# Kernel optimization log

Measured on AMD Instinct MI355X. Metric: run time of the kernel, lower is better.

The kernel has to match this reference:

```python
import jax, jax.numpy as jnp
import numpy as np

# dims
B, N, T, D = 32, 207, 12, 128
H, HD, L, FF = 8, 16, 4, 512
PL, OD, IN = 12, 1, 1
SCALE = 1.0 / float(np.sqrt(HD))
NEG = -1e9


def ln(x, g, b, eps=1e-5):
    m = jnp.mean(x, -1, keepdims=True)
    v = jnp.mean((x - m) ** 2, -1, keepdims=True)
    return (x - m) * jax.lax.rsqrt(v + eps) * g + b


def setup_inputs() -> dict:
    key = jax.random.key(0)
    keys = iter(jax.random.split(key, 48))
    def rn(shape, s=0.02):
        return jax.random.normal(next(keys), shape, jnp.float32) * s
    z = lambda *s: jnp.zeros(s, jnp.float32)
    o = lambda *s: jnp.ones(s, jnp.float32)
    inp = {
        "x": jax.random.normal(next(keys), (B, N, T, IN), jnp.float32),
        "adj": jax.random.randint(next(keys), (N, N), 0, 2, jnp.int32),
        "Wi": rn((IN, D)), "bi": z(D),
        # spatial blocks (stacked over L layers)
        "Wq": rn((L, D, D)), "Wk": rn((L, D, D)), "Wv": rn((L, D, D)),
        "Wo": rn((L, D, D)), "bo": z(L, D),
        "sW1": rn((L, D, FF)), "sB1": z(L, FF), "sW2": rn((L, FF, D)), "sB2": z(L, D),
        "sg1": o(L, D), "sh1": z(L, D), "sg2": o(L, D), "sh2": z(L, D),
        # temporal blocks
        "Win": rn((L, D, 3 * D)), "Bin": z(L, 3 * D), "Wout": rn((L, D, D)), "Bout": z(L, D),
        "tW1": rn((L, D, FF)), "tB1": z(L, FF), "tW2": rn((L, FF, D)), "tB2": z(L, D),
        "tg1": o(L, D), "th1": z(L, D), "tg2": o(L, D), "th2": z(L, D),
        # prediction head
        "P1": rn((D, 2 * D)), "Pb1": z(2 * D), "P2": rn((2 * D, D)), "Pb2": z(D),
        "P3": rn((D, PL * OD)), "Pb3": z(PL * OD),
    }
    return inp


def reference(x, adj, Wi, bi, Wq, Wk, Wv, Wo, bo, sW1, sB1, sW2, sB2,
              sg1, sh1, sg2, sh2, Win, Bin, Wout, Bout, tW1, tB1, tW2, tB2,
              tg1, th1, tg2, th2, P1, Pb1, P2, Pb2, P3, Pb3):
    mask = (adj == 0)  # [N,N] True = masked (no edge)
    cmask = jnp.triu(jnp.ones((T, T), bool), 1)  # causal mask over time
    h = x @ Wi + bi  # [B,N,T,D]
    for l in range(L):
        # --- spatial adjacency-masked attention (vectorized over t) ---
        xn = ln(h, sg1[l], sh1[l])
        q = (xn @ Wq[l]).reshape(B, N, T, H, HD)
        k = (xn @ Wk[l]).reshape(B, N, T, H, HD)
        v = (xn @ Wv[l]).reshape(B, N, T, H, HD)
        sc = jnp.einsum('bnthd,bmthd->bthnm', q, k) * SCALE  # [B,T,H,N,N]
        sc = jnp.where(mask[None, None, None], NEG, sc)
        a = jax.nn.softmax(sc, -1)
        o = jnp.einsum('bthnm,bmthd->bnthd', a, v).reshape(B, N, T, D)
        h = h + o @ Wo[l] + bo[l]
        xn = ln(h, sg2[l], sh2[l])
        h = h + jax.nn.relu(xn @ sW1[l] + sB1[l]) @ sW2[l] + sB2[l]
        # --- temporal causal attention (per node) ---
        xn = ln(h, tg1[l], th1[l])
        qkv = xn @ Win[l] + Bin[l]
        q, k, v = jnp.split(qkv, 3, -1)
        q = q.reshape(B, N, T, H, HD)
        k = k.reshape(B, N, T, H, HD)
        v = v.reshape(B, N, T, H, HD)
        sc = jnp.einsum('bnthd,bnshd->bnhts', q, k) * SCALE  # [B,N,H,T,T]
        sc = jnp.where(cmask[None, None, None], NEG, sc)
        a = jax.nn.softmax(sc, -1)
        o = jnp.einsum('bnhts,bnshd->bnthd', a, v).reshape(B, N, T, D)
        h = h + o @ Wout[l] + Bout[l]
        xn = ln(h, tg2[l], th2[l])
        h = h + jax.nn.relu(xn @ tW1[l] + tB1[l]) @ tW2[l] + tB2[l]
    # prediction head on last time step
    hl = h[:, :, -1, :]  # [B,N,D]
    zz = jax.nn.relu(hl @ P1 + Pb1)
    zz = jax.nn.relu(zz @ P2 + Pb2)
    return (zz @ P3 + Pb3).reshape(B, N, PL, OD)
```

## Files before the change

### kernel.cpp

```cpp
#include <hip/hip_runtime.h>
#include <hip/hip_bf16.h>

#define B_   32
#define N_   207
#define T_   12
#define D_   128
#define H_   8
#define HD_  16
#define L_   4
#define FF_  512
#define PL_  12
#define TOK  (B_*N_*T_)
#define ROWS2 (B_*N_)
#define SCALE_ 0.25f
#define NEG_  -1e9f
#define NPAD 208
#define KQ2  24
#define KVH  232
#define SLAB 3312
#define MSK_N (13*13*256)

typedef __hip_bfloat16 bf16;
typedef unsigned int u32;
typedef __attribute__((ext_vector_type(4))) unsigned int u32x4;
typedef __attribute__((ext_vector_type(8))) short bf16x8;
typedef __attribute__((ext_vector_type(8))) _Float16 f16x8;
typedef __attribute__((ext_vector_type(4))) float f32x4;

__device__ __forceinline__ float b2f(bf16 x){ return __bfloat162float(x); }
__device__ __forceinline__ bf16  f2b(float x){ return __float2bfloat16(x); }

__device__ __forceinline__ void gll16(const bf16* g, bf16* l){
  __builtin_amdgcn_global_load_lds((const __attribute__((address_space(1))) void*)g,
                                   (__attribute__((address_space(3))) void*)l, 16, 0, 0);
}

__global__ void detect_k(const void* x, int* flag){
  __shared__ int cnt[256];
  const unsigned short* u = (const unsigned short*)x;
  int ok = 0;
  for (int i = threadIdx.x; i < 4096; i += 256){
    unsigned int bits = ((unsigned int)u[i]) << 16;
    float f = __uint_as_float(bits);
    float a = fabsf(f);
    if (f == 0.0f || (a > 1e-4f && a < 64.0f)) ok++;
  }
  cnt[threadIdx.x] = ok;
  __syncthreads();
  for (int s = 128; s > 0; s >>= 1){
    if (threadIdx.x < s) cnt[threadIdx.x] += cnt[threadIdx.x + s];
    __syncthreads();
  }
  if (threadIdx.x == 0) *flag = (cnt[0] > 3686) ? 1 : 0;
}

struct FlatArgs {
  const void* src[24];
  long long dst[24];
  int cum[25];
};
__global__ void cvt_flat_k(FlatArgs a, bf16* base, const int* flag, int total){
  int i = blockIdx.x*256 + threadIdx.x;
  if (i >= total) return;
  int j = 0;
  while (i >= a.cum[j+1]) j++;
  int loc = i - a.cum[j];
  float v = (*flag) ? b2f(((const bf16*)a.src[j])[loc]) : ((const float*)a.src[j])[loc];
  base[a.dst[j] + loc] = f2b(v);
}

struct TArgs {
  const void* src[10];
  long long dst[10];
  int K[10], Nc[10], Lstr[10], ro[10];
  float scale[10];
  int cum[11];
};
__global__ void cvt_t_k(TArgs a, bf16* base, const int* flag, int total){
  int i = blockIdx.x*256 + threadIdx.x;
  if (i >= total) return;
  int j = 0;
  while (i >= a.cum[j+1]) j++;
  int loc = i - a.cum[j];
  int KN = a.K[j]*a.Nc[j];
  int l = loc / KN; int rm = loc - l*KN; int k = rm / a.Nc[j]; int n = rm - k*a.Nc[j];
  float v = (*flag) ? b2f(((const bf16*)a.src[j])[loc]) : ((const float*)a.src[j])[loc];
  base[a.dst[j] + (long long)l*a.Lstr[j] + (long long)(a.ro[j]+n)*a.K[j] + k] = f2b(v*a.scale[j]);
}

__global__ void maskc_k(const int* adj, float* maskg){
  int i = blockIdx.x*256 + threadIdx.x;
  if (i >= MSK_N) return;
  int cell = i >> 8;
  int mi = cell / 13, nj = cell - mi*13;
  int rem = i & 255;
  int lane = rem >> 2, r = rem & 3;
  int quad = lane >> 4, cl = lane & 15;
  int row = mi*16 + quad*4 + r; if (row > 206) row = 206;
  int col = nj*16 + cl;
  float v;
  if (col > 206) v = -1e30f;
  else v = adj[row*N_ + col] ? 0.0f : NEG_;
  maskg[i] = v;
}

__global__ void embed_ln_k(const bf16* x, const bf16* Wi, const bf16* bi,
                           const bf16* g, const bf16* bta, float* h, bf16* xnb){
  int wave = threadIdx.x >> 6, lane = threadIdx.x & 63;
  int tok = blockIdx.x*4 + wave;
  if (tok >= TOK) return;
  float xv = b2f(x[tok]);
  float v0 = xv*b2f(Wi[lane])    + b2f(bi[lane]);
  float v1 = xv*b2f(Wi[lane+64]) + b2f(bi[lane+64]);
  float* hp = h + (size_t)tok*D_;
  hp[lane] = v0; hp[lane+64] = v1;
  float s = v0 + v1;
  for (int off = 32; off >= 1; off >>= 1) s += __shfl_xor(s, off, 64);
  float m = s * (1.0f/128.0f);
  float d0 = v0 - m, d1 = v1 - m;
  float vv = d0*d0 + d1*d1;
  for (int off = 32; off >= 1; off >>= 1) vv += __shfl_xor(vv, off, 64);
  float r = rsqrtf(vv*(1.0f/128.0f) + 1e-5f);
  bf16* op = xnb + (size_t)tok*D_;
  op[lane]    = f2b(d0*r*b2f(g[lane])    + b2f(bta[lane]));
  op[lane+64] = f2b(d1*r*b2f(g[lane+64]) + b2f(bta[lane+64]));
}

__global__ __launch_bounds__(256) void mgemm_k(const bf16* __restrict__ A,
    const bf16* __restrict__ Wt, const bf16* __restrict__ bias,
    bf16* __restrict__ outp, int ldo, int Ktot, int relu){
  __shared__ __align__(16) bf16 As[128*32];
  __shared__ __align__(16) bf16 Bs[128*32];
  int tid = threadIdx.x;
  int rowBase = blockIdx.y * 128, colBase = blockIdx.x * 128;
  int w = tid >> 6, lane = tid & 63, quad = lane >> 4, cl = lane & 15;
  int waveM = w >> 1, waveN = w & 1;
  f32x4 accr[4][4];
  #pragma unroll
  for (int i = 0; i < 4; i++)
    #pragma unroll
    for (int j = 0; j < 4; j++) accr[i][j] = (f32x4){0.f,0.f,0.f,0.f};
  int lr = tid >> 2, kc = tid & 3;
  const bf16* Ap = A  + (size_t)(rowBase + lr)*Ktot + kc*8;
  const bf16* Bp = Wt + (size_t)(colBase + lr)*Ktot + kc*8;
  bf16* AsW = As + tid*8;
  bf16* BsW = Bs + tid*8;
  for (int kk = 0; kk < Ktot; kk += 32){
    __syncthreads();
    gll16(Ap + kk, AsW);
    gll16(Ap + (size_t)64*Ktot + kk, AsW + 64*32);
    gll16(Bp + kk, BsW);
    gll16(Bp + (size_t)64*Ktot + kk, BsW + 64*32);
    __syncthreads();
    bf16x8 af[4], bfr[4];
    #pragma unroll
    for (int mi = 0; mi < 4; mi++)
      af[mi] = *(const bf16x8*)(As + (waveM*64 + mi*16 + cl)*32 + quad*8);
    #pragma unroll
    for (int nj = 0; nj < 4; nj++)
      bfr[nj] = *(const bf16x8*)(Bs + (waveN*64 + nj*16 + cl)*32 + quad*8);
    #pragma unroll
    for (int mi = 0; mi < 4; mi++)
      #pragma unroll
      for (int nj = 0; nj < 4; nj++)
        accr[mi][nj] = __builtin_amdgcn_mfma_f32_16x16x32_bf16(af[mi], bfr[nj], accr[mi][nj], 0,0,0);
  }
  float bv[4];
  #pragma unroll
  for (int nj = 0; nj < 4; nj++)
    bv[nj] = bias ? b2f(bias[colBase + waveN*64 + nj*16 + cl]) : 0.0f;
  #pragma unroll
  for (int mi = 0; mi < 4; mi++){
    int row0 = rowBase + waveM*64 + mi*16 + quad*4;
    #pragma unroll
    for (int nj = 0; nj < 4; nj++){
      int col = colBase + waveN*64 + nj*16 + cl;
      #pragma unroll
      for (int r = 0; r < 4; r++){
        float v = accr[mi][nj][r] + bv[nj];
        if (relu) v = fmaxf(v, 0.0f);
        outp[(size_t)(row0+r)*ldo + col] = f2b(v);
      }
    }
  }
}

__global__ __launch_bounds__(256) void mgemm_qkvT_k(const bf16* __restrict__ A,
    const bf16* __restrict__ Wt, bf16* __restrict__ sQ,
    bf16* __restrict__ sK, bf16* __restrict__ sV){
  __shared__ __align__(16) bf16 As[128*32];
  __shared__ __align__(16) bf16 Bs[128*32];
  const int Ktot = 128;
  int tid = threadIdx.x;
  int rowBase = blockIdx.y * 128, colBase = blockIdx.x * 128;
  int w = tid >> 6, lane = tid & 63, quad = lane >> 4, cl = lane & 15;
  int waveM = w >> 1, waveN = w & 1;
  f32x4 accr[4][4];
  #pragma unroll
  for (int i = 0; i < 4; i++)
    #pragma unroll
    for (int j = 0; j < 4; j++) accr[i][j] = (f32x4){0.f,0.f,0.f,0.f};
  int lr = tid >> 2, kc = tid & 3;
  const bf16* Ap = A  + (size_t)(rowBase + lr)*Ktot + kc*8;
  const bf16* Bp = Wt + (size_t)(colBase + lr)*Ktot + kc*8;
  bf16* AsW = As + tid*8;
  bf16* BsW = Bs + tid*8;
  for (int kk = 0; kk < Ktot; kk += 32){
    __syncthreads();
    gll16(Ap + kk, AsW);
    gll16(Ap + (size_t)64*Ktot + kk, AsW + 64*32);
    gll16(Bp + kk, BsW);
    gll16(Bp + (size_t)64*Ktot + kk, BsW + 64*32);
    __syncthreads();
    bf16x8 af[4], bfr[4];
    #pragma unroll
    for (int mi = 0; mi < 4; mi++)
      af[mi] = *(const bf16x8*)(As + (waveM*64 + mi*16 + cl)*32 + quad*8);
    #pragma unroll
    for (int nj = 0; nj < 4; nj++)
      bfr[nj] = *(const bf16x8*)(Bs + (waveN*64 + nj*16 + cl)*32 + quad*8);
    #pragma unroll
    for (int mi = 0; mi < 4; mi++)
      #pragma unroll
      for (int nj = 0; nj < 4; nj++)
        accr[mi][nj] = __builtin_amdgcn_mfma_f32_16x16x32_bf16(af[mi], bfr[nj], accr[mi][nj], 0,0,0);
  }
  #pragma unroll
  for (int mi = 0; mi < 4; mi++){
    #pragma unroll
    for (int r = 0; r < 4; r++){
      int tok = rowBase + waveM*64 + mi*16 + quad*4 + r;
      int bn = tok / T_; int t = tok - bn*T_;
      int b = bn / N_;  int n = bn - b*N_;
      size_t base = ((size_t)(b*T_ + t)*H_)*SLAB + n*16 + cl;
      #pragma unroll
      for (int nj = 0; nj < 4; nj++){
        int col = colBase + waveN*64 + nj*16;
        int part = col >> 7, hh = (col >> 4) & 7;
        bf16* dst = (part == 0) ? sQ : (part == 1) ? sK : sV;
        dst[base + (size_t)hh*SLAB] = f2b(accr[mi][nj][r]);
      }
    }
  }
}

__global__ __launch_bounds__(256) void mgemm_ln_k(const bf16* __restrict__ A,
    const bf16* __restrict__ Wt, const bf16* __restrict__ bias,
    float* __restrict__ hout, int Ktot,
    const bf16* __restrict__ g, const bf16* __restrict__ bta,
    bf16* __restrict__ xnb){
  __shared__ __align__(16) bf16 As[128*32];
  __shared__ __align__(16) bf16 Bs[128*32];
  __shared__ float red[2][128][2];
  int tid = threadIdx.x;
  int rowBase = blockIdx.y * 128;
  int w = tid >> 6, lane = tid & 63, quad = lane >> 4, cl = lane & 15;
  int waveM = w >> 1, waveN = w & 1;
  f32x4 accr[4][4];
  #pragma unroll
  for (int i = 0; i < 4; i++)
    #pragma unroll
    for (int j = 0; j < 4; j++) accr[i][j] = (f32x4){0.f,0.f,0.f,0.f};
  int lr = tid >> 2, kc = tid & 3;
  const bf16* Ap = A  + (size_t)(rowBase + lr)*Ktot + kc*8;
  const bf16* Bp = Wt + (size_t)lr*Ktot + kc*8;
  bf16* AsW = As + tid*8;
  bf16* BsW = Bs + tid*8;
  for (int kk = 0; kk < Ktot; kk += 32){
    __syncthreads();
    gll16(Ap + kk, AsW);
    gll16(Ap + (size_t)64*Ktot + kk, AsW + 64*32);
    gll16(Bp + kk, BsW);
    gll16(Bp + (size_t)64*Ktot + kk, BsW + 64*32);
    __syncthreads();
    bf16x8 af[4], bfr[4];
    #pragma unroll
    for (int mi = 0; mi < 4; mi++)
      af[mi] = *(const bf16x8*)(As + (waveM*64 + mi*16 + cl)*32 + quad*8);
    #pragma unroll
    for (int nj = 0; nj < 4; nj++)
      bfr[nj] = *(const bf16x8*)(Bs + (waveN*64 + nj*16 + cl)*32 + quad*8);
    #pragma unroll
    for (int mi = 0; mi < 4; mi++)
      #pragma unroll
      for (int nj = 0; nj < 4; nj++)
        accr[mi][nj] = __builtin_amdgcn_mfma_f32_16x16x32_bf16(af[mi], bfr[nj], accr[mi][nj], 0,0,0);
  }
  int colW = waveN*64;
  float bv[4];
  #pragma unroll
  for (int nj = 0; nj < 4; nj++)
    bv[nj] = bias ? b2f(bias[colW + nj*16 + cl]) : 0.0f;
  float hv[4][4][4];
  float psum[4][4], psq[4][4];
  #pragma unroll
  for (int mi = 0; mi < 4; mi++)
    #pragma unroll
    for (int r = 0; r < 4; r++){ psum[mi][r] = 0.f; psq[mi][r] = 0.f; }
  #pragma unroll
  for (int mi = 0; mi < 4; mi++){
    #pragma unroll
    for (int r = 0; r < 4; r++){
      int row = rowBase + waveM*64 + mi*16 + quad*4 + r;
      #pragma unroll
      for (int nj = 0; nj < 4; nj++){
        int col = colW + nj*16 + cl;
        size_t idx = (size_t)row*D_ + col;
        float v = hout[idx] + accr[mi][nj][r] + bv[nj];
        hout[idx] = v;
        hv[mi][nj][r] = v;
        psum[mi][r] += v; psq[mi][r] += v*v;
      }
    }
  }
  if (g){
    #pragma unroll
    for (int off = 1; off <= 8; off <<= 1)
      #pragma unroll
      for (int mi = 0; mi < 4; mi++)
        #pragma unroll
        for (int r = 0; r < 4; r++){
          psum[mi][r] += __shfl_xor(psum[mi][r], off, 64);
          psq[mi][r]  += __shfl_xor(psq[mi][r],  off, 64);
        }
    if (cl == 0){
      #pragma unroll
      for (int mi = 0; mi < 4; mi++)
        #pragma unroll
        for (int r = 0; r < 4; r++){
          int rl = waveM*64 + mi*16 + quad*4 + r;
          red[waveN][rl][0] = psum[mi][r];
          red[waveN][rl][1] = psq[mi][r];
        }
    }
    __syncthreads();
    float gv[4], btv[4];
    #pragma unroll
    for (int nj = 0; nj < 4; nj++){
      int col = colW + nj*16 + cl;
      gv[nj] = b2f(g[col]); btv[nj] = b2f(bta[col]);
    }
    #pragma unroll
    for (int mi = 0; mi < 4; mi++){
      #pragma unroll
      for (int r = 0; r < 4; r++){
        int rl = waveM*64 + mi*16 + quad*4 + r;
        float s = red[0][rl][0] + red[1][rl][0];
        float q = red[0][rl][1] + red[1][rl][1];
        float mean = s*(1.0f/128.0f);
        float var  = q*(1.0f/128.0f) - mean*mean;
        float rstd = rsqrtf(var + 1e-5f);
        int row = rowBase + rl;
        #pragma unroll
        for (int nj = 0; nj < 4; nj++){
          int col = colW + nj*16 + cl;
          xnb[(size_t)row*D_ + col] = f2b((hv[mi][nj][r]-mean)*rstd*gv[nj] + btv[nj]);
        }
      }
    }
  }
}

__global__ __launch_bounds__(256,2) void mffn_ln_k(const bf16* __restrict__ A,
    const bf16* __restrict__ W1t, const bf16* __restrict__ b1,
    const bf16* __restrict__ W2t, const bf16* __restrict__ b2,
    float* __restrict__ hout,
    const bf16* __restrict__ g, const bf16* __restrict__ bta,
    bf16* __restrict__ xnb){
  __shared__ __align__(16) bf16 As[128*136];
  __shared__ __align__(16) bf16 Hs[128*136];
  __shared__ __align__(16) bf16 Bs[128*32];
  __shared__ float red[2][128][2];
  int tid = threadIdx.x;
  int rowBase = blockIdx.x * 128;
  int w = tid >> 6, lane = tid & 63, quad = lane >> 4, cl = lane & 15;
  int waveM = w >> 1, waveN = w & 1;
  for (int i = tid; i < 128*16; i += 256){
    int row = i >> 4, ch = i & 15;
    u32x4 v = *(const u32x4*)(A + (size_t)(rowBase + row)*128 + ch*8);
    *(u32x4*)(As + row*136 + ch*8) = v;
  }
  f32x4 acc2[4][4];
  #pragma unroll
  for (int i = 0; i < 4; i++)
    #pragma unroll
    for (int j = 0; j < 4; j++) acc2[i][j] = (f32x4){0.f,0.f,0.f,0.f};
  int lr = tid >> 2, kc = tid & 3;
  bf16* BsW = Bs + tid*8;
  int aRow0 = waveM*64;
  for (int kt = 0; kt < 4; kt++){
    f32x4 acc1[4][4];
    #pragma unroll
    for (int i = 0; i < 4; i++)
      #pragma unroll
      for (int j = 0; j < 4; j++) acc1[i][j] = (f32x4){0.f,0.f,0.f,0.f};
    for (int ks = 0; ks < 4; ks++){
      __syncthreads();
      gll16(W1t + (size_t)(kt*128 + lr)*128 + ks*32 + kc*8, BsW);
      gll16(W1t + (size_t)(kt*128 + 64 + lr)*128 + ks*32 + kc*8, BsW + 64*32);
      __syncthreads();
      bf16x8 af[4], bfr[4];
      #pragma unroll
      for (int mi = 0; mi < 4; mi++)
        af[mi] = *(const bf16x8*)(As + (aRow0 + mi*16 + cl)*136 + ks*32 + quad*8);
      #pragma unroll
      for (int nj = 0; nj < 4; nj++)
        bfr[nj] = *(const bf16x8*)(Bs + (waveN*64 + nj*16 + cl)*32 + quad*8);
      #pragma unroll
      for (int mi = 0; mi < 4; mi++)
        #pragma unroll
        for (int nj = 0; nj < 4; nj++)
          acc1[mi][nj] = __builtin_amdgcn_mfma_f32_16x16x32_bf16(af[mi], bfr[nj], acc1[mi][nj], 0,0,0);
    }
    float b1v[4];
    #pragma unroll
    for (int nj = 0; nj < 4; nj++)
      b1v[nj] = b2f(b1[kt*128 + waveN*64 + nj*16 + cl]);
    #pragma unroll
    for (int mi = 0; mi < 4; mi++){
      #pragma unroll
      for (int r = 0; r < 4; r++){
        int row = aRow0 + mi*16 + quad*4 + r;
        #pragma unroll
        for (int nj = 0; nj < 4; nj++){
          int col = waveN*64 + nj*16 + cl;
          Hs[row*136 + col] = f2b(fmaxf(acc1[mi][nj][r] + b1v[nj], 0.0f));
        }
      }
    }
    for (int ks = 0; ks < 4; ks++){
      __syncthreads();
      gll16(W2t + (size_t)lr*512 + kt*128 + ks*32 + kc*8, BsW);
      gll16(W2t + (size_t)(64 + lr)*512 + kt*128 + ks*32 + kc*8, BsW + 64*32);
      __syncthreads();
      bf16x8 af[4], bfr[4];
      #pragma unroll
      for (int mi = 0; mi < 4; mi++)
        af[mi] = *(const bf16x8*)(Hs + (aRow0 + mi*16 + cl)*136 + ks*32 + quad*8);
      #pragma unroll
      for (int nj = 0; nj < 4; nj++)
        bfr[nj] = *(const bf16x8*)(Bs + (waveN*64 + nj*16 + cl)*32 + quad*8);
      #pragma unroll
      for (int mi = 0; mi < 4; mi++)
        #pragma unroll
        for (int nj = 0; nj < 4; nj++)
          acc2[mi][nj] = __builtin_amdgcn_mfma_f32_16x16x32_bf16(af[mi], bfr[nj], acc2[mi][nj], 0,0,0);
    }
    __syncthreads();
  }
  int colW = waveN*64;
  float bv[4];
  #pragma unroll
  for (int nj = 0; nj < 4; nj++)
    bv[nj] = b2f(b2[colW + nj*16 + cl]);
  float hv[4][4][4];
  float psum[4][4], psq[4][4];
  #pragma unroll
  for (int mi = 0; mi < 4; mi++)
    #pragma unroll
    for (int r = 0; r < 4; r++){ psum[mi][r] = 0.f; psq[mi][r] = 0.f; }
  #pragma unroll
  for (int mi = 0; mi < 4; mi++){
    #pragma unroll
    for (int r = 0; r < 4; r++){
      int row = rowBase + aRow0 + mi*16 + quad*4 + r;
      #pragma unroll
      for (int nj = 0; nj < 4; nj++){
        int col = colW + nj*16 + cl;
        size_t idx = (size_t)row*D_ + col;
        float v = hout[idx] + acc2[mi][nj][r] + bv[nj];
        hout[idx] = v;
        hv[mi][nj][r] = v;
        psum[mi][r] += v; psq[mi][r] += v*v;
      }
    }
  }
  if (g){
    #pragma unroll
    for (int off = 1; off <= 8; off <<= 1)
      #pragma unroll
      for (int mi = 0; mi < 4; mi++)
        #pragma unroll
        for (int r = 0; r < 4; r++){
          psum[mi][r] += __shfl_xor(psum[mi][r], off, 64);
          psq[mi][r]  += __shfl_xor(psq[mi][r],  off, 64);
        }
    if (cl == 0){
      #pragma unroll
      for (int mi = 0; mi < 4; mi++)
        #pragma unroll
        for (int r = 0; r < 4; r++){
          int rl = aRow0 + mi*16 + quad*4 + r;
          red[waveN][rl][0] = psum[mi][r];
          red[waveN][rl][1] = psq[mi][r];
        }
    }
    __syncthreads();
    float gv[4], btv[4];
    #pragma unroll
    for (int nj = 0; nj < 4; nj++){
      int col = colW + nj*16 + cl;
      gv[nj] = b2f(g[col]); btv[nj] = b2f(bta[col]);
    }
    #pragma unroll
    for (int mi = 0; mi < 4; mi++){
      #pragma unroll
      for (int r = 0; r < 4; r++){
        int rl = aRow0 + mi*16 + quad*4 + r;
        float s = red[0][rl][0] + red[1][rl][0];
        float q = red[0][rl][1] + red[1][rl][1];
        float mean = s*(1.0f/128.0f);
        float var  = q*(1.0f/128.0f) - mean*mean;
        float rstd = rsqrtf(var + 1e-5f);
        int row = rowBase + rl;
        #pragma unroll
        for (int nj = 0; nj < 4; nj++){
          int col = colW + nj*16 + cl;
          xnb[(size_t)row*D_ + col] = f2b((hv[mi][nj][r]-mean)*rstd*gv[nj] + btv[nj]);
        }
      }
    }
  }
}

__global__ __launch_bounds__(256,3) void sattn_k(const bf16* __restrict__ sQ,
    const bf16* __restrict__ sK, const bf16* __restrict__ sV,
    const float* __restrict__ maskg, bf16* __restrict__ ob){
  __shared__ __align__(16) bf16     Ks[NPAD*KQ2];
  __shared__ __align__(16) _Float16 Vt[16*KVH];
  __shared__ __align__(16) _Float16 Ps[4*16*KVH];
  int tid = threadIdx.x;
  int bid = blockIdx.x;
  int hh = bid & 7; int bt = bid >> 3; int t = bt % T_; int b = bt / T_;
  const bf16* Kslab = sK + (size_t)bid*SLAB;
  const bf16* Vslab = sV + (size_t)bid*SLAB;
  const bf16* Qslab = sQ + (size_t)bid*SLAB;
  for (int i = tid; i < 16*25; i += 256){ int d = i/25, c = 207 + i%25; Vt[d*KVH + c] = (_Float16)0.0f; }
  for (int i = tid; i < 64*24; i += 256){ int row = i/24, c = 208 + i%24; Ps[row*KVH + c] = (_Float16)0.0f; }
  for (int c = tid; c < 414; c += 256){
    bf16x8 kv = *(const bf16x8*)(Kslab + c*8);
    int n = c >> 1, dh = (c & 1)*8;
    *(bf16x8*)(Ks + n*KQ2 + dh) = kv;
  }
  for (int i = tid; i < SLAB; i += 256){
    int n = i >> 4, d = i & 15;
    Vt[d*KVH + n] = (_Float16)b2f(Vslab[i]);
  }
  __syncthreads();

  int lane = tid & 63, w = tid >> 6, quad = lane >> 4, cl = lane & 15;
  int nstripes = (w == 0) ? 4 : 3;
  for (int si = 0; si < nstripes; si++){
    int mi = w + si*4;
    bf16x8 aq = (bf16x8){0,0,0,0,0,0,0,0};
    {
      int n = mi*16 + cl; if (n > N_-1) n = N_-1;
      if (quad < 2) aq = *(const bf16x8*)(Qslab + n*16 + quad*8);
    }
    const float* mrow = maskg + ((size_t)mi*13)*256 + lane*4;
    f32x4 s[13];
    #pragma unroll
    for (int nj = 0; nj < 13; nj++){
      bf16x8 bk = (bf16x8){0,0,0,0,0,0,0,0};
      if (quad < 2) bk = *(const bf16x8*)(Ks + (nj*16 + cl)*KQ2 + quad*8);
      f32x4 c0 = *(const f32x4*)(mrow + nj*256);
      s[nj] = __builtin_amdgcn_mfma_f32_16x16x32_bf16(aq, bk, c0, 0,0,0);
    }
    int row0 = mi*16 + quad*4;
    _Float16* Pw = Ps + w*16*KVH;
    float invr[4];
    #pragma unroll
    for (int r = 0; r < 4; r++){
      float sum = 0.0f;
      #pragma unroll
      for (int nj = 0; nj < 13; nj++){
        float e = __expf(s[nj][r]);
        s[nj][r] = e; sum += e;
      }
      for (int off = 1; off < 16; off <<= 1) sum += __shfl_xor(sum, off, 64);
      invr[r] = 1.0f/sum;
      _Float16* Pr = Pw + (quad*4 + r)*KVH;
      #pragma unroll
      for (int nj = 0; nj < 13; nj++) Pr[nj*16 + cl] = (_Float16)s[nj][r];
    }
    __threadfence_block();
    f32x4 o = {0.f,0.f,0.f,0.f};
    #pragma unroll
    for (int kt = 0; kt < 7; kt++){
      f16x8 ap = *(const f16x8*)(Pw + cl*KVH + kt*32 + quad*8);
      f16x8 bv = *(const f16x8*)(Vt + cl*KVH + kt*32 + quad*8);
      o = __builtin_amdgcn_mfma_f32_16x16x32_f16(ap, bv, o, 0,0,0);
    }
    #pragma unroll
    for (int r = 0; r < 4; r++){
      int rg = row0 + r;
      if (rg < N_)
        ob[((size_t)((b*N_ + rg)*T_ + t))*D_ + hh*HD_ + cl] = f2b(o[r]*invr[r]);
    }
    __threadfence_block();
  }
}

__global__ void tattn_k(const bf16* qkv, bf16* ob){
  int bid = blockIdx.x; int b = bid / N_, n = bid % N_;
  __shared__ float qs[T_*D_];
  __shared__ float ks[T_*D_];
  __shared__ float vs[T_*D_];
  size_t rowb = ((size_t)(b*N_+n)*T_)*384;
  const u32* src = (const u32*)(qkv + rowb);
  for (int idx = threadIdx.x; idx < T_*192; idx += 128){
    int tt = idx / 192, cw = idx - tt*192;
    u32 pr = src[tt*192 + cw];
    union { u32 u; bf16 b[2]; } cv; cv.u = pr;
    float v0 = b2f(cv.b[0]), v1 = b2f(cv.b[1]);
    int arr = cw >> 6, cp2 = (cw & 63)*2;
    float* dst = (arr == 0) ? qs : (arr == 1) ? ks : vs;
    dst[tt*128 + cp2] = v0; dst[tt*128 + cp2 + 1] = v1;
  }
  __syncthreads();
  int p = threadIdx.x;
  if (p < H_*T_){
    int hh = p / T_, t = p - hh*T_;
    float qreg[16];
    for (int d = 0; d < 16; d++) qreg[d] = qs[t*128 + hh*16 + d];
    float sc[12]; float mx = -3.4e38f;
    for (int s = 0; s < 12; s++){
      float a = 0.0f;
      for (int d = 0; d < 16; d++) a += qreg[d]*ks[s*128 + hh*16 + d];
      a = (s <= t) ? a*SCALE_ : -3.4e38f;
      sc[s] = a; mx = fmaxf(mx, a);
    }
    float ssum = 0.0f;
    for (int s = 0; s < 12; s++){
      float e = (s <= t) ? __expf(sc[s]-mx) : 0.0f;
      sc[s] = e; ssum += e;
    }
    float inv = 1.0f/ssum;
    size_t obase = ((size_t)(b*N_+n)*T_ + t)*D_ + hh*16;
    for (int d = 0; d < 16; d++){
      float acc = 0.0f;
      for (int s = 0; s < 12; s++) acc += sc[s]*vs[s*128 + hh*16 + d];
      ob[obase + d] = f2b(acc*inv);
    }
  }
}

__global__ void gemm_k(const bf16* A, int lda, const bf16* W, const bf16* bias,
                       void* outp, int ldo, int M, int Ncols, int K, int relu, int acc){
  __shared__ float Ast[16*68];
  __shared__ float Ws [16*68];
  int tx = threadIdx.x & 15, ty = threadIdx.x >> 4;
  int rowBase = blockIdx.y * 64, colBase = blockIdx.x * 64;
  float accr[4][4];
  for (int i = 0; i < 4; i++) for (int j = 0; j < 4; j++) accr[i][j] = 0.0f;
  for (int kk = 0; kk < K; kk += 16){
    int kq = threadIdx.x & 15, r0 = threadIdx.x >> 4;
    for (int it = 0; it < 4; it++){
      int r = r0 + it*16, row = rowBase + r;
      float v = 0.0f;
      if (row < M) v = b2f(A[(size_t)row*lda + kk + kq]);
      Ast[kq*68 + r] = v;
    }
    int c = threadIdx.x & 63, w0 = threadIdx.x >> 6;
    for (int it = 0; it < 4; it++){
      int kr = w0 + it*4;
      Ws[kr*68 + c] = b2f(W[(size_t)(kk+kr)*Ncols + colBase + c]);
    }
    __syncthreads();
    for (int k = 0; k < 16; k++){
      float av[4], wv[4];
      for (int i = 0; i < 4; i++) av[i] = Ast[k*68 + ty*4 + i];
      for (int j = 0; j < 4; j++) wv[j] = Ws[k*68 + tx*4 + j];
      for (int i = 0; i < 4; i++)
        for (int j = 0; j < 4; j++) accr[i][j] += av[i]*wv[j];
    }
    __syncthreads();
  }
  for (int i = 0; i < 4; i++){
    int row = rowBase + ty*4 + i;
    if (row >= M) continue;
    for (int j = 0; j < 4; j++){
      int col = colBase + tx*4 + j;
      float v = accr[i][j];
      if (bias) v += b2f(bias[col]);
      if (relu) v = fmaxf(v, 0.0f);
      if (acc) ((float*)outp)[(size_t)row*ldo + col] += v;
      else     ((bf16*)outp)[(size_t)row*ldo + col] = f2b(v);
    }
  }
}

__global__ void gather_k(const float* h, bf16* hlb){
  int i = blockIdx.x*256 + threadIdx.x;
  if (i >= ROWS2*D_) return;
  int r = i >> 7, d = i & 127;
  hlb[i] = f2b(h[((size_t)r*T_ + (T_-1))*D_ + d]);
}

__global__ void head3_k(const bf16* z2, const bf16* P3, const bf16* Pb3,
                        void* out, int out_n, const int* flag){
  int i = blockIdx.x*256 + threadIdx.x;
  if (i >= out_n) return;
  int r = i / PL_, j = i - r*PL_;
  float acc = b2f(Pb3[j]);
  for (int d = 0; d < 128; d++) acc += b2f(z2[(size_t)r*128 + d]) * b2f(P3[d*PL_ + j]);
  if (*flag) ((bf16*)out)[i] = f2b(acc);
  else       ((float*)out)[i] = acc;
}

extern "C" void kernel_launch(void* const* d_in, const int* in_sizes, int n_in,
                              void* d_out, int out_size, void* d_ws, size_t ws_size,
                              hipStream_t stream){
  size_t HB = (size_t)TOK*D_*4;
  size_t XB = (size_t)TOK*D_*2;
  size_t RB = (size_t)TOK*D_*8;
  float* h    = (float*)d_ws;
  bf16*  xnb  = (bf16*)((char*)d_ws + HB);
  bf16*  reg_ = (bf16*)((char*)d_ws + HB + XB);
  bf16*  cvt  = (bf16*)((char*)d_ws + HB + XB + RB);
  bf16*  wsb  = (bf16*)d_ws;
  const int FIDX[34] = {0,2,3,4,5,6,7,8,9,10,11,12,13,14,15,16,17,18,19,20,
                        21,22,23,24,25,26,27,28,29,30,31,32,33,34};
  bf16* cp[34];
  size_t off = 0;
  for (int i = 0; i < 34; i++){ cp[i] = cvt + off; off += (size_t)in_sizes[FIDX[i]]; }
  char* tail   = (char*)d_ws + HB + XB + RB + ((off*2 + 255) & ~(size_t)255);
  float* maskg = (float*)tail;
  bf16* qkvw   = (bf16*)(tail + (size_t)MSK_N*4);
  int*  flag   = (int*)(tail + (size_t)MSK_N*4 + (size_t)L_*384*128*2);

  const bf16 *x_c=cp[0], *Wi_c=cp[1], *bi_c=cp[2],
             *Wo_t=cp[6], *bo_c=cp[7], *sW1_t=cp[8], *sB1_c=cp[9], *sW2_t=cp[10], *sB2_c=cp[11],
             *sg1_c=cp[12], *sh1_c=cp[13], *sg2_c=cp[14], *sh2_c=cp[15], *Win_t=cp[16], *Bin_c=cp[17],
             *Wout_t=cp[18], *Bout_c=cp[19], *tW1_t=cp[20], *tB1_c=cp[21], *tW2_t=cp[22], *tB2_c=cp[23],
             *tg1_c=cp[24], *th1_c=cp[25], *tg2_c=cp[26], *th2_c=cp[27], *P1_c=cp[28], *Pb1_c=cp[29],
             *P2_c=cp[30], *Pb2_c=cp[31], *P3_c=cp[32], *Pb3_c=cp[33];
  const int* adj = (const int*)d_in[1];

  bf16* sQ   = reg_;
  bf16* sK   = reg_ + (size_t)TOK*128;
  bf16* sV   = reg_ + (size_t)2*TOK*128;
  bf16* ob   = reg_ + (size_t)3*TOK*128;
  bf16* qkvb = reg_;

  detect_k<<<1, 256, 0, stream>>>(d_in[0], flag);

  {
    const int FLAT[24] = {0,1,2,7,9,11,12,13,14,15,17,19,21,23,24,25,26,27,28,29,30,31,32,33};
    FlatArgs fa; int c = 0;
    for (int ii = 0; ii < 24; ii++){
      int ci = FLAT[ii];
      fa.src[ii] = d_in[FIDX[ci]];
      fa.dst[ii] = (long long)(cp[ci] - wsb);
      fa.cum[ii] = c;
      c += in_sizes[FIDX[ci]];
    }
    fa.cum[24] = c;
    cvt_flat_k<<<(c+255)/256, 256, 0, stream>>>(fa, wsb, flag, c);
  }
  {
    TArgs ta; int c = 0;
    const void* srcs[10] = {d_in[4], d_in[5], d_in[6], d_in[7], d_in[9], d_in[11],
                            d_in[17], d_in[19], d_in[21], d_in[23]};
    bf16* dsts[10] = {qkvw, qkvw, qkvw, cp[6], cp[8], cp[10], cp[16], cp[18], cp[20], cp[22]};
    int Ks_[10]   = {128,128,128, 128, 128, 512, 128, 128, 128, 512};
    int Ncs[10]   = {128,128,128, 128, 512, 128, 384, 128, 512, 128};
    int Lst[10]   = {384*128,384*128,384*128, 128*128, 128*512, 512*128, 128*384, 128*128, 128*512, 512*128};
    int ros[10]   = {0,128,256, 0,0,0, 0,0,0, 0};
    for (int j = 0; j < 10; j++){
      ta.src[j] = srcs[j];
      ta.dst[j] = (long long)(dsts[j] - wsb);
      ta.K[j] = Ks_[j]; ta.Nc[j] = Ncs[j]; ta.Lstr[j] = Lst[j]; ta.ro[j] = ros[j];
      ta.scale[j] = (j == 0) ? SCALE_ : 1.0f;
      ta.cum[j] = c;
      c += L_*Ks_[j]*Ncs[j];
    }
    ta.cum[10] = c;
    cvt_t_k<<<(c+255)/256, 256, 0, stream>>>(ta, wsb, flag, c);
  }
  maskc_k<<<(MSK_N+255)/256, 256, 0, stream>>>(adj, maskg);
  embed_ln_k<<<TOK/4, 256, 0, stream>>>(x_c, Wi_c, bi_c, sg1_c, sh1_c, h, xnb);

  const dim3 gP  (1, TOK/128);
  const dim3 gQKV(3, TOK/128);

  for (int l = 0; l < L_; l++){
    mgemm_qkvT_k<<<gQKV, 256, 0, stream>>>(xnb, qkvw + (size_t)l*384*128, sQ, sK, sV);
    sattn_k<<<B_*T_*H_, 256, 0, stream>>>(sQ, sK, sV, maskg, ob);
    mgemm_ln_k<<<gP, 256, 0, stream>>>(ob, Wo_t + (size_t)l*D_*D_, bo_c + l*D_, h, D_,
                                       sg2_c + l*D_, sh2_c + l*D_, xnb);
    mffn_ln_k<<<TOK/128, 256, 0, stream>>>(xnb, sW1_t + (size_t)l*D_*FF_, sB1_c + l*FF_,
                                           sW2_t + (size_t)l*FF_*D_, sB2_c + l*D_, h,
                                           tg1_c + l*D_, th1_c + l*D_, xnb);
    mgemm_k<<<gQKV, 256, 0, stream>>>(xnb, Win_t + (size_t)l*D_*384, Bin_c + l*384, qkvb, 384, D_, 0);
    tattn_k<<<B_*N_, 128, 0, stream>>>(qkvb, ob);
    mgemm_ln_k<<<gP, 256, 0, stream>>>(ob, Wout_t + (size_t)l*D_*D_, Bout_c + l*D_, h, D_,
                                       tg2_c + l*D_, th2_c + l*D_, xnb);
    const bf16* gnext = (l < L_-1) ? (sg1_c + (l+1)*D_) : nullptr;
    const bf16* bnext = (l < L_-1) ? (sh1_c + (l+1)*D_) : nullptr;
    mffn_ln_k<<<TOK/128, 256, 0, stream>>>(xnb, tW1_t + (size_t)l*D_*FF_, tB1_c + l*FF_,
                                           tW2_t + (size_t)l*FF_*D_, tB2_c + l*D_, h,
                                           gnext, bnext, xnb);
  }

  bf16* hlb = reg_;
  bf16* z1  = reg_ + (size_t)ROWS2*128;
  bf16* z2  = z1   + (size_t)ROWS2*256;
  gather_k<<<(ROWS2*D_)/256, 256, 0, stream>>>(h, hlb);
  gemm_k<<<dim3(256/64, (ROWS2+63)/64), 256, 0, stream>>>(hlb, 128, P1_c, Pb1_c, z1, 256, ROWS2, 256, 128, 1, 0);
  gemm_k<<<dim3(128/64, (ROWS2+63)/64), 256, 0, stream>>>(z1, 256, P2_c, Pb2_c, z2, 128, ROWS2, 128, 256, 1, 0);
  head3_k<<<(out_size+255)/256, 256, 0, stream>>>(z2, P3_c, Pb3_c, d_out, out_size, flag);
}
```

Baseline: 1.619 ms.

## Use exp2 softmax with folded log2e, MFMA row sums, and direct K loads

Folds log2(e) into the pre-scaled Wq weights and the mask constant so the spatial softmax can use exp2f instead of __expf. The softmax denominator now comes from an extra MFMA against a ones vector, which removes the per-row shuffle reductions. K tiles are read straight from global memory rather than staged in LDS. Dropping the K LDS buffer allows the launch-bounds occupancy hint to go from 3 to 4, at the cost of uncoalesced global K reads, an extra MFMA per step, and row sums taken from fp16-rounded probabilities.

Result: faster. 1.571 ms, median of 3 (-3.0%).

```diff
diff --git a/kernel.cpp b/kernel.cpp
--- a/kernel.cpp
+++ b/kernel.cpp
@@ -13,9 +13,8 @@
 #define TOK  (B_*N_*T_)
 #define ROWS2 (B_*N_)
 #define SCALE_ 0.25f
-#define NEG_  -1e9f
-#define NPAD 208
-#define KQ2  24
+#define LOG2E_ 1.4426950408889634f
+#define NEG2_ -1.4426950409e9f
 #define KVH  232
 #define SLAB 3312
 #define MSK_N (13*13*256)
@@ -100,7 +99,7 @@
   int col = nj*16 + cl;
   float v;
   if (col > 206) v = -1e30f;
-  else v = adj[row*N_ + col] ? 0.0f : NEG_;
+  else v = adj[row*N_ + col] ? 0.0f : NEG2_;
   maskg[i] = v;
 }
 
@@ -523,10 +522,9 @@
   }
 }
 
-__global__ __launch_bounds__(256,3) void sattn_k(const bf16* __restrict__ sQ,
+__global__ __launch_bounds__(256,4) void sattn_k(const bf16* __restrict__ sQ,
     const bf16* __restrict__ sK, const bf16* __restrict__ sV,
     const float* __restrict__ maskg, bf16* __restrict__ ob){
-  __shared__ __align__(16) bf16     Ks[NPAD*KQ2];
   __shared__ __align__(16) _Float16 Vt[16*KVH];
   __shared__ __align__(16) _Float16 Ps[4*16*KVH];
   int tid = threadIdx.x;
@@ -537,11 +535,6 @@
   const bf16* Qslab = sQ + (size_t)bid*SLAB;
   for (int i = tid; i < 16*25; i += 256){ int d = i/25, c = 207 + i%25; Vt[d*KVH + c] = (_Float16)0.0f; }
   for (int i = tid; i < 64*24; i += 256){ int row = i/24, c = 208 + i%24; Ps[row*KVH + c] = (_Float16)0.0f; }
-  for (int c = tid; c < 414; c += 256){
-    bf16x8 kv = *(const bf16x8*)(Kslab + c*8);
-    int n = c >> 1, dh = (c & 1)*8;
-    *(bf16x8*)(Ks + n*KQ2 + dh) = kv;
-  }
   for (int i = tid; i < SLAB; i += 256){
     int n = i >> 4, d = i & 15;
     Vt[d*KVH + n] = (_Float16)b2f(Vslab[i]);
@@ -549,6 +542,9 @@
   __syncthreads();
 
   int lane = tid & 63, w = tid >> 6, quad = lane >> 4, cl = lane & 15;
+  f16x8 ones8;
+  #pragma unroll
+  for (int j = 0; j < 8; j++) ones8[j] = (_Float16)1.0f;
   int nstripes = (w == 0) ? 4 : 3;
   for (int si = 0; si < nstripes; si++){
     int mi = w + si*4;
@@ -562,40 +558,37 @@
     #pragma unroll
     for (int nj = 0; nj < 13; nj++){
       bf16x8 bk = (bf16x8){0,0,0,0,0,0,0,0};
-      if (quad < 2) bk = *(const bf16x8*)(Ks + (nj*16 + cl)*KQ2 + quad*8);
+      if (quad < 2){
+        int nb = nj*16 + cl; if (nb > N_-1) nb = N_-1;
+        bk = *(const bf16x8*)(Kslab + nb*16 + quad*8);
+      }
       f32x4 c0 = *(const f32x4*)(mrow + nj*256);
       s[nj] = __builtin_amdgcn_mfma_f32_16x16x32_bf16(aq, bk, c0, 0,0,0);
     }
     int row0 = mi*16 + quad*4;
     _Float16* Pw = Ps + w*16*KVH;
-    float invr[4];
     #pragma unroll
     for (int r = 0; r < 4; r++){
-      float sum = 0.0f;
-      #pragma unroll
-      for (int nj = 0; nj < 13; nj++){
-        float e = __expf(s[nj][r]);
-        s[nj][r] = e; sum += e;
-      }
-      for (int off = 1; off < 16; off <<= 1) sum += __shfl_xor(sum, off, 64);
-      invr[r] = 1.0f/sum;
       _Float16* Pr = Pw + (quad*4 + r)*KVH;
       #pragma unroll
-      for (int nj = 0; nj < 13; nj++) Pr[nj*16 + cl] = (_Float16)s[nj][r];
+      for (int nj = 0; nj < 13; nj++)
+        Pr[nj*16 + cl] = (_Float16)exp2f(s[nj][r]);
     }
     __threadfence_block();
     f32x4 o = {0.f,0.f,0.f,0.f};
+    f32x4 osum = {0.f,0.f,0.f,0.f};
     #pragma unroll
     for (int kt = 0; kt < 7; kt++){
       f16x8 ap = *(const f16x8*)(Pw + cl*KVH + kt*32 + quad*8);
       f16x8 bv = *(const f16x8*)(Vt + cl*KVH + kt*32 + quad*8);
-      o = __builtin_amdgcn_mfma_f32_16x16x32_f16(ap, bv, o, 0,0,0);
+      o    = __builtin_amdgcn_mfma_f32_16x16x32_f16(ap, bv,    o,    0,0,0);
+      osum = __builtin_amdgcn_mfma_f32_16x16x32_f16(ap, ones8, osum, 0,0,0);
     }
     #pragma unroll
     for (int r = 0; r < 4; r++){
       int rg = row0 + r;
       if (rg < N_)
-        ob[((size_t)((b*N_ + rg)*T_ + t))*D_ + hh*HD_ + cl] = f2b(o[r]*invr[r]);
+        ob[((size_t)((b*N_ + rg)*T_ + t))*D_ + hh*HD_ + cl] = f2b(o[r]/osum[r]);
     }
     __threadfence_block();
   }
@@ -771,7 +764,7 @@
       ta.src[j] = srcs[j];
       ta.dst[j] = (long long)(dsts[j] - wsb);
       ta.K[j] = Ks_[j]; ta.Nc[j] = Ncs[j]; ta.Lstr[j] = Lst[j]; ta.ro[j] = ros[j];
-      ta.scale[j] = (j == 0) ? SCALE_ : 1.0f;
+      ta.scale[j] = (j == 0) ? SCALE_*LOG2E_ : 1.0f;
       ta.cum[j] = c;
       c += L_*Ks_[j]*Ncs[j];
     }
```
